# Kernel optimization log

Hardware: AMD Instinct MI355X
Metric: run time of the kernel (lower is better)

## Reference

```python
import jax, jax.numpy as jnp
import numpy as np

B, S, D, H = 4, 127, 768, 12
HD = D // H
NS = S + 1
GAMMA = 1.0
NEG_INF = -1e9
EPS = 1e-6


def setup_inputs() -> dict:
    key = jax.random.key(0)
    ks = jax.random.split(key, 12)
    s = 0.02
    return {
        'desc': jax.random.normal(ks[0], (B, S, D), jnp.float32),
        'nve': jax.random.normal(ks[1], (B, NS, D), jnp.float32),
        'mask_M': jax.random.uniform(ks[2], (B, H, S, S), jnp.float32),
        'Wq': jax.random.normal(ks[3], (D, D), jnp.float32) * s,
        'bq': jnp.zeros((D,), jnp.float32),
        'Wk': jax.random.normal(ks[4], (D, D), jnp.float32) * s,
        'bk': jnp.zeros((D,), jnp.float32),
        'Wv': jax.random.normal(ks[5], (D, D), jnp.float32) * s,
        'bv': jnp.zeros((D,), jnp.float32),
        'eW1': jax.random.normal(ks[6], (2 * D, D), jnp.float32) * s,
        'eb1': jnp.zeros((D,), jnp.float32),
        'ln_g': jnp.ones((D,), jnp.float32),
        'ln_b': jnp.zeros((D,), jnp.float32),
        'eW2': jax.random.normal(ks[7], (D, D), jnp.float32) * s,
        'eb2': jnp.zeros((D,), jnp.float32),
        'aW': jax.random.normal(ks[8], (3 * HD,), jnp.float32) * s,
        'ab': jnp.zeros((), jnp.float32),
    }


def _layernorm(x, g, b):
    m = jnp.mean(x, -1, keepdims=True)
    v = jnp.var(x, -1, keepdims=True)
    return (x - m) * jax.lax.rsqrt(v + 1e-5) * g + b


def _adjacency():
    # CLS->Var on, Var->CLS off, Var-Var without self loop
    var_adj = 1.0 - jnp.eye(S, dtype=jnp.float32)
    adj = jnp.zeros((NS, NS), jnp.float32)
    adj = adj.at[1:, 1:].set(var_adj)
    adj = adj.at[0, 1:].set(1.0)
    return adj  # [NS, NS]


def reference(desc, nve, mask_M, Wq, bq, Wk, bk, Wv, bv, eW1, eb1, ln_g, ln_b, eW2, eb2, aW, ab):
    adj = _adjacency()

    def proj(W, bias):
        return (nve @ W + bias).reshape(B, NS, H, HD).transpose(0, 2, 1, 3)  # [B,H,NS,HD]

    q, k, v = proj(Wq, bq), proj(Wk, bk), proj(Wv, bv)

    # edge features: pairwise concat of desc embeddings, CLS edges = [desc, desc]
    node_i = jnp.broadcast_to(desc[:, :, None, :], (B, S, S, D))
    node_j = jnp.broadcast_to(desc[:, None, :, :], (B, S, S, D))
    var_edge = jnp.concatenate([node_i, node_j], -1)           # [B,S,S,2D]
    cls_edge = jnp.concatenate([desc, desc], -1)               # [B,S,2D]
    edge = jnp.zeros((B, NS, NS, 2 * D), jnp.float32)
    edge = edge.at[:, 1:, 1:].set(var_edge)
    edge = edge.at[:, 0, 1:].set(cls_edge)
    edge = edge.at[:, 1:, 0].set(cls_edge)

    # edge_update MLP: Linear -> LayerNorm -> ReLU -> Linear
    h = jax.nn.relu(_layernorm(edge @ eW1 + eb1, ln_g, ln_b))
    e = h @ eW2 + eb2                                           # [B,NS,NS,D]
    e = e.reshape(B, NS, NS, H, HD).transpose(0, 3, 1, 2, 4)    # [B,H,NS,NS,HD]
    e = e * adj[None, None, :, :, None]

    # attn_proj on concat([q_i, k_j, e_ij]) == sum of three dot products + bias
    aq, ak, ae = aW[:HD], aW[HD:2 * HD], aW[2 * HD:]
    logits = (jnp.einsum('bhid,d->bhi', q, aq)[:, :, :, None]
              + jnp.einsum('bhjd,d->bhj', k, ak)[:, :, None, :]
              + jnp.einsum('bhijd,d->bhij', e, ae) + ab)        # [B,H,NS,NS]

    # logit bias from Var-Var probabilities
    p = jnp.clip(mask_M, EPS, 1.0 - EPS)
    bias = (jnp.log(p) - jnp.log(1.0 - p)) * GAMMA
    logits = logits.at[:, :, 1:, 1:].add(bias)

    logits = logits + jnp.where(adj == 0.0, NEG_INF, 0.0)[None, None]
    attn = jax.nn.softmax(logits, axis=-1)                      # dropout off (eval)
    context = jnp.einsum('bhij,bhjd->bhid', attn, v)
    basis_outputs = context.transpose(0, 2, 1, 3)               # [B,NS,H,HD]
    return basis_outputs, attn
```

## Files before the change

kernel.cpp:

```cpp
#include <hip/hip_runtime.h>
#include <hip/hip_bf16.h>

#define BB  4
#define SS  127
#define DD  768
#define HH  12
#define HDl 64
#define NSl 128

typedef __attribute__((ext_vector_type(8))) short short8;
typedef __attribute__((ext_vector_type(4))) float f32x4;

constexpr int OFF_P   = 0;
constexpr int OFF_Q   = OFF_P  + BB*SS*DD;
constexpr int OFF_V   = OFF_Q  + BB*SS*DD;
constexpr int OFF_QA  = OFF_V  + BB*NSl*DD;
constexpr int OFF_KA  = OFF_QA + BB*NSl*HH;
constexpr int OFF_W2B = OFF_KA + BB*NSl*HH;
constexpr int OFF_WQA = OFF_W2B + 6144;
constexpr int OFF_WKA = OFF_WQA + HH*DD;
constexpr int OFF_BF  = OFF_WKA + HH*DD;
constexpr int OFF_EL  = OFF_BF + 64;

__device__ inline unsigned short f2bf(float f) {
    unsigned int u = __builtin_bit_cast(unsigned int, f);
    u += 0x7fffu + ((u >> 16) & 1u);
    return (unsigned short)(u >> 16);
}

__device__ inline short8 pack8(float4 a, float4 b) {
    short8 p;
    p[0] = (short)f2bf(a.x); p[1] = (short)f2bf(a.y);
    p[2] = (short)f2bf(a.z); p[3] = (short)f2bf(a.w);
    p[4] = (short)f2bf(b.x); p[5] = (short)f2bf(b.y);
    p[6] = (short)f2bf(b.z); p[7] = (short)f2bf(b.w);
    return p;
}

__device__ inline void unpack8(short8 s, float* f) {
    int4 u = __builtin_bit_cast(int4, s);
    f[0] = __builtin_bit_cast(float, u.x << 16);
    f[1] = __builtin_bit_cast(float, u.x & 0xffff0000);
    f[2] = __builtin_bit_cast(float, u.y << 16);
    f[3] = __builtin_bit_cast(float, u.y & 0xffff0000);
    f[4] = __builtin_bit_cast(float, u.z << 16);
    f[5] = __builtin_bit_cast(float, u.z & 0xffff0000);
    f[6] = __builtin_bit_cast(float, u.w << 16);
    f[7] = __builtin_bit_cast(float, u.w & 0xffff0000);
}

__device__ inline unsigned int cvtpk(float lo, float hi) {
    unsigned int r;
    asm volatile("v_cvt_pk_bf16_f32 %0, %1, %2" : "=v"(r) : "v"(lo), "v"(hi));
    return r;
}

constexpr int NB_PQ   = 96;
constexpr int NB_V    = 96;
constexpr int FOLD_T  = 3 * HH * DD + 36 + 4 * DD;
constexpr int NB_FOLD = (FOLD_T + 511) / 512;

__global__ __launch_bounds__(512) void mega1(
        const float* __restrict__ desc, const float* __restrict__ nve,
        const float* __restrict__ eW1, const float* __restrict__ Wv,
        const float* __restrict__ bv, const float* __restrict__ eb1,
        const float* __restrict__ Wq, const float* __restrict__ Wk,
        const float* __restrict__ eW2,
        const float* __restrict__ bq, const float* __restrict__ bk,
        const float* __restrict__ eb2, const float* __restrict__ aW,
        unsigned short* __restrict__ Pu, unsigned short* __restrict__ Qu,
        unsigned short* __restrict__ Vu,
        unsigned short* __restrict__ W2Bu, float* __restrict__ WQA,
        float* __restrict__ WKA, float* __restrict__ bfold) {
    const int bid = blockIdx.x;
    const int tid = threadIdx.x;

    if (bid >= NB_PQ + NB_V) {
        int idx = (bid - NB_PQ - NB_V) * 512 + tid;
        const int total = 3 * HH * DD;
        if (idx < total) {
            int which = idx / (HH * DD);
            int r = idx % (HH * DD);
            int h = r / DD;
            int c = r % DD;
            const float* W = (which == 0) ? eW2 : (which == 1) ? Wq : Wk;
            const float* a = (which == 0) ? (aW + 2 * HDl) : (which == 1) ? aW : (aW + HDl);
            float s = 0.f;
            #pragma unroll 8
            for (int d = 0; d < HDl; ++d) s += W[c * DD + h * HDl + d] * a[d];
            if (which == 0) W2Bu[h * DD + c] = f2bf(s);
            else if (which == 1) WQA[h * DD + c] = s;
            else WKA[h * DD + c] = s;
        } else if (idx < total + 36) {
            int r = idx - total;
            int which = r / HH, h = r % HH;
            const float* bb = (which == 0) ? eb2 : (which == 1) ? bq : bk;
            const float* a = (which == 0) ? (aW + 2 * HDl) : (which == 1) ? aW : (aW + HDl);
            float s = 0.f;
            for (int d = 0; d < HDl; ++d) s += bb[h * HDl + d] * a[d];
            bfold[r] = s;
        } else if (idx < FOLD_T) {
            W2Bu[12 * DD + (idx - total - 36)] = 0;
        }
        return;
    }

    const bool pq = (bid < NB_PQ);
    const int r = pq ? bid : bid - NB_PQ;
    const int bcol = (r % 12) * 64;
    const int brow = (r / 12) * 64;
    const float* A  = pq ? desc : nve;
    const float* B0 = pq ? eW1 : Wv;
    const int M = pq ? (BB * SS) : (BB * NSl);

    __shared__ short lds[3 * 64 * 64];
    short* As  = lds;
    short* Bs0 = lds + 4096;
    short* Bs1 = lds + 8192;

    const int arow = tid >> 3, akc = (tid & 7) * 8;
    const int abyte = (arow * 128 + akc * 2) ^ ((arow & 7) << 4);
    const int bn = tid & 63, bg = tid >> 6;
    const int bbyte = (bn * 128 + bg * 16) ^ ((bn & 7) << 4);

    const int gm = brow + arow;
    const float* arow_p = A + gm * DD + akc;

    short8 gA, gB0, gB1;
    auto loadA = [&](int k0) {
        float4 f0 = {0,0,0,0}, f1 = {0,0,0,0};
        if (gm < M) {
            f0 = *(const float4*)(arow_p + k0);
            f1 = *(const float4*)(arow_p + k0 + 4);
        }
        gA = pack8(f0, f1);
    };
    auto loadB = [&](const float* Bm, int k0, short8& dst) {
        float v[8];
        #pragma unroll
        for (int q = 0; q < 8; ++q)
            v[q] = Bm[(k0 + bg * 8 + q) * DD + bcol + bn];
        short8 p;
        #pragma unroll
        for (int q = 0; q < 8; ++q) p[q] = (short)f2bf(v[q]);
        dst = p;
    };

    loadA(0);
    loadB(B0, 0, gB0);
    if (pq) loadB(eW1 + DD * DD, 0, gB1);

    const int lane = tid & 63;
    const int w = tid >> 6;
    const int wr = w >> 1, wc = w & 1;
    const int l15 = lane & 15;

    f32x4 acc0[2] = {};
    f32x4 acc1[2] = {};

    for (int k0 = 0; k0 < DD; k0 += 64) {
        *(short8*)((char*)As + abyte) = gA;
        *(short8*)((char*)Bs0 + bbyte) = gB0;
        if (pq) *(short8*)((char*)Bs1 + bbyte) = gB1;
        __syncthreads();
        if (k0 + 64 < DD) {
            loadA(k0 + 64);
            loadB(B0, k0 + 64, gB0);
            if (pq) loadB(eW1 + DD * DD, k0 + 64, gB1);
        }
        #pragma unroll
        for (int ks = 0; ks < 2; ++ks) {
            const int kb = ks * 64 + ((lane >> 4) << 4);
            int row = wr * 16 + l15;
            short8 af = *(const short8*)((char*)As + ((row * 128 + kb) ^ ((row & 7) << 4)));
            #pragma unroll
            for (int ni = 0; ni < 2; ++ni) {
                int col = wc * 32 + ni * 16 + l15;
                int cb = (col * 128 + kb) ^ ((col & 7) << 4);
                short8 b0 = *(const short8*)((char*)Bs0 + cb);
                acc0[ni] = __builtin_amdgcn_mfma_f32_16x16x32_bf16(af, b0, acc0[ni], 0, 0, 0);
                if (pq) {
                    short8 b1 = *(const short8*)((char*)Bs1 + cb);
                    acc1[ni] = __builtin_amdgcn_mfma_f32_16x16x32_bf16(af, b1, acc1[ni], 0, 0, 0);
                }
            }
        }
        __syncthreads();
    }

    #pragma unroll
    for (int ni = 0; ni < 2; ++ni) {
        int gcol = bcol + wc * 32 + ni * 16 + l15;
        float bias0 = pq ? 0.f : bv[gcol];
        float bias1 = pq ? eb1[gcol] : 0.f;
        #pragma unroll
        for (int rr = 0; rr < 4; ++rr) {
            int grow = brow + wr * 16 + ((lane >> 4) << 2) + rr;
            if (grow < M) {
                if (pq) {
                    Pu[grow * DD + gcol] = f2bf(acc0[ni][rr]);
                    Qu[grow * DD + gcol] = f2bf(acc1[ni][rr] + bias1);
                } else {
                    Vu[grow * DD + gcol] = f2bf(acc0[ni][rr] + bias0);
                }
            }
        }
    }
}

__global__ __launch_bounds__(512) void pairqk_kernel(
        const unsigned short* __restrict__ Pu, const unsigned short* __restrict__ Qu,
        const float* __restrict__ nve,
        const float* __restrict__ ln_g, const float* __restrict__ ln_b,
        const unsigned short* __restrict__ W2Bu,
        const float* __restrict__ WQA, const float* __restrict__ WKA,
        const float* __restrict__ bfold,
        float* __restrict__ qa, float* __restrict__ ka,
        float* __restrict__ e_log) {
    __shared__ short pB[16 * 768];
    __shared__ short qB[16 * 768];
    __shared__ float gbl[2 * 768];
    __shared__ float2 pstat[16];
    __shared__ float2 qstat[16];

    const int tid = threadIdx.x;

    if (blockIdx.z >= BB) {
        int qb = (blockIdx.z - BB) * 64 + blockIdx.y * 8 + blockIdx.x;
        int wid = qb * 8 + (tid >> 6);
        int lane = tid & 63;
        int which = wid & 1;
        int r = wid >> 1;
        int h = r % HH;
        int t = (r / HH) % NSl;
        int b = r / (HH * NSl);
        const float* W = (which ? WKA : WQA) + h * DD;
        const float* row = nve + (b * NSl + t) * DD;
        float s = 0.f;
        #pragma unroll
        for (int rr = 0; rr < 12; ++rr) {
            int c = lane + 64 * rr;
            s += row[c] * W[c];
        }
        #pragma unroll
        for (int off = 32; off; off >>= 1) s += __shfl_xor(s, off);
        if (lane == 0)
            (which ? ka : qa)[(b * NSl + t) * HH + h] = s + bfold[12 + which * 12 + h];
        return;
    }

    const int b   = blockIdx.z;
    const int pi0 = blockIdx.y * 16, qj0 = blockIdx.x * 16;

    {
        int row = tid >> 5;
        int ccb = tid & 31;
        const unsigned short* psrc = Pu + (b * SS + min(pi0 + row, SS - 1)) * DD;
        const unsigned short* qsrc = Qu + (b * SS + min(qj0 + row, SS - 1)) * DD;
        float ps = 0.f, pss = 0.f, qs = 0.f, qss = 0.f;
        float f[8];
        #pragma unroll
        for (int it = 0; it < 3; ++it) {
            int cc = ccb + it * 32;
            int byte = (row * 1536 + cc * 16) ^ ((row & 7) << 4);
            short8 pv = *(const short8*)(psrc + cc * 8);
            unpack8(pv, f);
            #pragma unroll
            for (int q = 0; q < 8; ++q) { ps += f[q]; pss += f[q] * f[q]; }
            *(short8*)((char*)pB + byte) = pv;
            short8 qv = *(const short8*)(qsrc + cc * 8);
            unpack8(qv, f);
            #pragma unroll
            for (int q = 0; q < 8; ++q) { qs += f[q]; qss += f[q] * f[q]; }
            *(short8*)((char*)qB + byte) = qv;
        }
        #pragma unroll
        for (int off = 16; off; off >>= 1) {
            ps  += __shfl_xor(ps, off);
            pss += __shfl_xor(pss, off);
            qs  += __shfl_xor(qs, off);
            qss += __shfl_xor(qss, off);
        }
        if ((tid & 31) == 0) {
            pstat[tid >> 5] = make_float2(ps, pss);
            qstat[tid >> 5] = make_float2(qs, qss);
        }
    }
    if (tid < 384) {
        int c = tid * 4;
        float4 v = (tid < 192) ? *(const float4*)(ln_g + c)
                               : *(const float4*)(ln_b + (c - 768));
        *(float4*)(gbl + c) = v;
    }
    __syncthreads();

    const int lane = tid & 63;
    const int w    = tid >> 6;
    const int l15  = lane & 15;
    const int kg   = lane >> 4;

    f32x4 gacc = {};
    #pragma unroll 4
    for (int ks = 0; ks < 24; ++ks) {
        int cb = ks * 64 + kg * 16;
        short8 ap = *(const short8*)((char*)pB + ((l15 * 1536 + cb) ^ ((l15 & 7) << 4)));
        short8 aq = *(const short8*)((char*)qB + ((l15 * 1536 + cb) ^ ((l15 & 7) << 4)));
        gacc = __builtin_amdgcn_mfma_f32_16x16x32_bf16(ap, aq, gacc, 0, 0, 0);
    }

    float al[2], be[2];
    #pragma unroll
    for (int s = 0; s < 2; ++s) {
        int pl = 2 * w + s;
        int src = ((pl >> 2) << 4) | l15;
        int rsel = pl & 3;
        float gg = (rsel == 0) ? gacc[0] : (rsel == 1) ? gacc[1]
                 : (rsel == 2) ? gacc[2] : gacc[3];
        gg = __shfl(gg, src);
        float2 pst = pstat[pl];
        float2 qst = qstat[l15];
        float mean = (pst.x + qst.x) * (1.f / DD);
        float sumsq = pst.y + 2.f * gg + qst.y;
        float var = sumsq * (1.f / DD) - mean * mean;
        float a = rsqrtf(var + 1e-5f);
        al[s] = a;
        be[s] = -mean * a;
    }

    const unsigned short* wrow = W2Bu + l15 * 768;
    const int r0 = 2 * w, r1 = 2 * w + 1;
    const int p0base = r0 * 1536, p1base = r1 * 1536;
    const int p0x = (r0 & 7) << 4, p1x = (r1 & 7) << 4;
    f32x4 acc0 = {}, acc1 = {};

    #pragma unroll 2
    for (int ks = 0; ks < 24; ++ks) {
        const int c0 = ks * 32 + kg * 8;
        short8 bfg = *(const short8*)(wrow + c0);
        f32x4 g0 = *(const f32x4*)(gbl + c0);
        f32x4 g1 = *(const f32x4*)(gbl + c0 + 4);
        f32x4 bb0 = *(const f32x4*)(gbl + 768 + c0);
        f32x4 bb1 = *(const f32x4*)(gbl + 768 + c0 + 4);
        float gv[8] = {g0.x, g0.y, g0.z, g0.w, g1.x, g1.y, g1.z, g1.w};
        float bv8[8] = {bb0.x, bb0.y, bb0.z, bb0.w, bb1.x, bb1.y, bb1.z, bb1.w};

        short8 q8 = *(const short8*)((char*)qB + ((l15 * 1536 + c0 * 2) ^ ((l15 & 7) << 4)));
        float qf[8];
        unpack8(q8, qf);

        short8 p8 = *(const short8*)((char*)pB + ((p0base + c0 * 2) ^ p0x));
        float pf[8];
        unpack8(p8, pf);
        float y[8];
        #pragma unroll
        for (int j = 0; j < 8; ++j) {
            float t = pf[j] + qf[j];
            float u = __builtin_fmaf(al[0], t, be[0]);
            y[j] = fmaxf(__builtin_fmaf(gv[j], u, bv8[j]), 0.f);
        }
        {
            int4 ti = { (int)cvtpk(y[0], y[1]), (int)cvtpk(y[2], y[3]),
                        (int)cvtpk(y[4], y[5]), (int)cvtpk(y[6], y[7]) };
            short8 ya = __builtin_bit_cast(short8, ti);
            acc0 = __builtin_amdgcn_mfma_f32_16x16x32_bf16(ya, bfg, acc0, 0, 0, 0);
        }

        p8 = *(const short8*)((char*)pB + ((p1base + c0 * 2) ^ p1x));
        unpack8(p8, pf);
        #pragma unroll
        for (int j = 0; j < 8; ++j) {
            float t = pf[j] + qf[j];
            float u = __builtin_fmaf(al[1], t, be[1]);
            y[j] = fmaxf(__builtin_fmaf(gv[j], u, bv8[j]), 0.f);
        }
        {
            int4 ti = { (int)cvtpk(y[0], y[1]), (int)cvtpk(y[2], y[3]),
                        (int)cvtpk(y[4], y[5]), (int)cvtpk(y[6], y[7]) };
            short8 ya = __builtin_bit_cast(short8, ti);
            acc1 = __builtin_amdgcn_mfma_f32_16x16x32_bf16(ya, bfg, acc1, 0, 0, 0);
        }
    }

    if (l15 < HH) {
        const float badd = bfold[l15];
        #pragma unroll
        for (int s = 0; s < 2; ++s) {
            int pig = pi0 + 2 * w + s;
            if (pig >= SS) continue;
            f32x4 A = s ? acc1 : acc0;
            #pragma unroll
            for (int r = 0; r < 4; ++r) {
                int qjg = qj0 + (kg << 2) + r;
                if (qjg < SS) {
                    int i = (pig == qjg) ? 0 : (pig + 1);
                    e_log[(((b * HH + l15) * NSl) + i) * NSl + (qjg + 1)] = A[r] + badd;
                }
            }
        }
    }
}

__global__ __launch_bounds__(512) void softmax_ctx_kernel(
        const float* __restrict__ e_log,
        const float* __restrict__ qa, const float* __restrict__ ka,
        const float* __restrict__ mask_M, const float* __restrict__ ab,
        const unsigned short* __restrict__ Vu,
        float* __restrict__ out) {
    __shared__ short Vt[64 * 128];
    __shared__ short plb[32 * 128];
    __shared__ float kal[NSl];

    const int b = blockIdx.z;
    const int h = blockIdx.y;
    const int iq = blockIdx.x;
    const int tid = threadIdx.x;
    const int lane = tid & 63;
    const int w = tid >> 6;

    {
        int j = tid >> 2;
        int dq = (tid & 3) * 16;
        const unsigned short* src = Vu + (b * NSl + j) * DD + h * HDl + dq;
        short8 s0 = *(const short8*)(src);
        short8 s1 = *(const short8*)(src + 8);
        #pragma unroll
        for (int t = 0; t < 8; ++t) {
            int d = dq + t;
            *(short*)((char*)Vt + ((d * 256 + j * 2) ^ ((d & 7) << 4))) = s0[t];
        }
        #pragma unroll
        for (int t = 0; t < 8; ++t) {
            int d = dq + 8 + t;
            *(short*)((char*)Vt + ((d * 256 + j * 2) ^ ((d & 7) << 4))) = s1[t];
        }
    }
    if (tid < NSl) kal[tid] = ka[(b * NSl + tid) * HH + h];
    __syncthreads();

    const float abv = ab[0];

    for (int rr = 0; rr < 4; ++rr) {
        const int il = w * 4 + rr;
        const int i = iq * 32 + il;
        const float qv = qa[(b * NSl + i) * HH + h];
        const float* e_row = e_log + (((b * HH + h) * NSl) + i) * NSl;

        float lg[2];
        bool valid[2];
        #pragma unroll
        for (int s = 0; s < 2; ++s) {
            int j = 1 + lane + 64 * s;
            bool v = (j < NSl) && !(i >= 1 && j == i);
            float l = -1e30f;
            if (v) {
                l = e_row[j] + qv + kal[j] + abv;
                if (i >= 1) {
                    float p = mask_M[((b * HH + h) * SS + (i - 1)) * SS + (j - 1)];
                    p = fminf(fmaxf(p, 1e-6f), 1.0f - 1e-6f);
                    l += __logf(p / (1.0f - p));
                }
            }
            lg[s] = l;
            valid[s] = v;
        }
        float m = fmaxf(lg[0], lg[1]);
        #pragma unroll
        for (int off = 32; off; off >>= 1) m = fmaxf(m, __shfl_xor(m, off));
        float e0 = valid[0] ? __expf(lg[0] - m) : 0.f;
        float e1 = valid[1] ? __expf(lg[1] - m) : 0.f;
        float s = e0 + e1;
        #pragma unroll
        for (int off = 32; off; off >>= 1) s += __shfl_xor(s, off);
        const float inv = 1.0f / s;

        const float p0 = e0 * inv, p1 = e1 * inv;

        float* attn_row = out + BB * NSl * HH * HDl + (((b * HH + h) * NSl) + i) * NSl;
        attn_row[1 + lane] = p0;
        if (65 + lane < NSl) attn_row[65 + lane] = p1;
        if (lane == 0) attn_row[0] = 0.f;

        {
            int byte0 = (il * 256 + (1 + lane) * 2) ^ ((il & 7) << 4);
            *(short*)((char*)plb + byte0) = (short)f2bf(p0);
            if (65 + lane < NSl) {
                int byte1 = (il * 256 + (65 + lane) * 2) ^ ((il & 7) << 4);
                *(short*)((char*)plb + byte1) = (short)f2bf(p1);
            }
            if (lane == 0) {
                int byteZ = (il * 256) ^ ((il & 7) << 4);
                *(short*)((char*)plb + byteZ) = 0;
            }
        }
    }
    __syncthreads();

    const int l15 = lane & 15;
    const int kg  = lane >> 4;
    const int itile = w >> 2, dtile = w & 3;
    const int arow  = itile * 16 + l15;
    const int bcold = dtile * 16 + l15;
    f32x4 acc = {};
    #pragma unroll
    for (int ks = 0; ks < 4; ++ks) {
        int kb = (ks * 32 + kg * 8) * 2;
        short8 af = *(const short8*)((char*)plb + ((arow * 256 + kb) ^ ((arow & 7) << 4)));
        short8 bf = *(const short8*)((char*)Vt  + ((bcold * 256 + kb) ^ ((bcold & 7) << 4)));
        acc = __builtin_amdgcn_mfma_f32_16x16x32_bf16(af, bf, acc, 0, 0, 0);
    }
    #pragma unroll
    for (int r = 0; r < 4; ++r) {
        int i = iq * 32 + itile * 16 + kg * 4 + r;
        out[((b * NSl + i) * HH + h) * HDl + dtile * 16 + l15] = acc[r];
    }
}

extern "C" void kernel_launch(void* const* d_in, const int* in_sizes, int n_in,
                              void* d_out, int out_size, void* d_ws, size_t ws_size,
                              hipStream_t stream) {
    const float* desc   = (const float*)d_in[0];
    const float* nve    = (const float*)d_in[1];
    const float* mask_M = (const float*)d_in[2];
    const float* Wq     = (const float*)d_in[3];
    const float* bq     = (const float*)d_in[4];
    const float* Wk     = (const float*)d_in[5];
    const float* bk     = (const float*)d_in[6];
    const float* Wv     = (const float*)d_in[7];
    const float* bv     = (const float*)d_in[8];
    const float* eW1    = (const float*)d_in[9];
    const float* eb1    = (const float*)d_in[10];
    const float* ln_g   = (const float*)d_in[11];
    const float* ln_b   = (const float*)d_in[12];
    const float* eW2    = (const float*)d_in[13];
    const float* eb2    = (const float*)d_in[14];
    const float* aW     = (const float*)d_in[15];
    const float* ab     = (const float*)d_in[16];

    float* ws  = (float*)d_ws;
    float* out = (float*)d_out;
    unsigned short* Pu   = (unsigned short*)(ws + OFF_P);
    unsigned short* Qu   = (unsigned short*)(ws + OFF_Q);
    unsigned short* Vu   = (unsigned short*)(ws + OFF_V);
    unsigned short* W2Bu = (unsigned short*)(ws + OFF_W2B);

    mega1<<<NB_PQ + NB_V + NB_FOLD, 512, 0, stream>>>(
        desc, nve, eW1, Wv, bv, eb1,
        Wq, Wk, eW2, bq, bk, eb2, aW,
        Pu, Qu, Vu,
        W2Bu, ws + OFF_WQA, ws + OFF_WKA, ws + OFF_BF);

    pairqk_kernel<<<dim3(8, 8, BB + 24), 512, 0, stream>>>(
        Pu, Qu, nve, ln_g, ln_b, W2Bu,
        ws + OFF_WQA, ws + OFF_WKA, ws + OFF_BF,
        ws + OFF_QA, ws + OFF_KA, ws + OFF_EL);

    softmax_ctx_kernel<<<dim3(4, HH, BB), 512, 0, stream>>>(
        ws + OFF_EL, ws + OFF_QA, ws + OFF_KA, mask_M, ab, Vu, out);
}
```

Before: 52.53 us.

## Double-buffer mega1 GEMM prefetch and split softmax_ctx into smaller blocks

```diff
diff --git a/kernel.cpp b/kernel.cpp
--- a/kernel.cpp
+++ b/kernel.cpp
@@ -111,12 +111,10 @@
     const int brow = (r / 12) * 64;
     const float* A  = pq ? desc : nve;
     const float* B0 = pq ? eW1 : Wv;
+    const float* B1 = eW1 + DD * DD;
     const int M = pq ? (BB * SS) : (BB * NSl);
 
-    __shared__ short lds[3 * 64 * 64];
-    short* As  = lds;
-    short* Bs0 = lds + 4096;
-    short* Bs1 = lds + 8192;
+    __shared__ short lds[2 * 3 * 4096];
 
     const int arow = tid >> 3, akc = (tid & 7) * 8;
     const int abyte = (arow * 128 + akc * 2) ^ ((arow & 7) << 4);
@@ -126,14 +124,13 @@
     const int gm = brow + arow;
     const float* arow_p = A + gm * DD + akc;
 
-    short8 gA, gB0, gB1;
-    auto loadA = [&](int k0) {
+    auto loadA = [&](int k0, short8& dst) {
         float4 f0 = {0,0,0,0}, f1 = {0,0,0,0};
         if (gm < M) {
             f0 = *(const float4*)(arow_p + k0);
             f1 = *(const float4*)(arow_p + k0 + 4);
         }
-        gA = pack8(f0, f1);
+        dst = pack8(f0, f1);
     };
     auto loadB = [&](const float* Bm, int k0, short8& dst) {
         float v[8];
@@ -146,9 +143,9 @@
         dst = p;
     };
 
-    loadA(0);
-    loadB(B0, 0, gB0);
-    if (pq) loadB(eW1 + DD * DD, 0, gB1);
+    short8 sA[2], sB0[2], sB1[2];
+    loadA(0, sA[0]);  loadB(B0, 0, sB0[0]);  if (pq) loadB(B1, 0, sB1[0]);
+    loadA(64, sA[1]); loadB(B0, 64, sB0[1]); if (pq) loadB(B1, 64, sB1[1]);
 
     const int lane = tid & 63;
     const int w = tid >> 6;
@@ -158,16 +155,24 @@
     f32x4 acc0[2] = {};
     f32x4 acc1[2] = {};
 
-    for (int k0 = 0; k0 < DD; k0 += 64) {
-        *(short8*)((char*)As + abyte) = gA;
-        *(short8*)((char*)Bs0 + bbyte) = gB0;
-        if (pq) *(short8*)((char*)Bs1 + bbyte) = gB1;
+    for (int k = 0; k < 12; ++k) {
+        const int p = k & 1;
+        short* As  = lds + p * 12288;
+        short* Bs0 = As + 4096;
+        short* Bs1 = As + 8192;
+
+        *(short8*)((char*)As + abyte)  = sA[p];
+        *(short8*)((char*)Bs0 + bbyte) = sB0[p];
+        if (pq) *(short8*)((char*)Bs1 + bbyte) = sB1[p];
         __syncthreads();
-        if (k0 + 64 < DD) {
-            loadA(k0 + 64);
-            loadB(B0, k0 + 64, gB0);
-            if (pq) loadB(eW1 + DD * DD, k0 + 64, gB1);
-        }
+
+        if (k + 2 < 12) {
+            int k0 = (k + 2) * 64;
+            loadA(k0, sA[p]);
+            loadB(B0, k0, sB0[p]);
+            if (pq) loadB(B1, k0, sB1[p]);
+        }
+
         #pragma unroll
         for (int ks = 0; ks < 2; ++ks) {
             const int kb = ks * 64 + ((lane >> 4) << 4);
@@ -400,14 +405,14 @@
     }
 }
 
-__global__ __launch_bounds__(512) void softmax_ctx_kernel(
+__global__ __launch_bounds__(256) void softmax_ctx_kernel(
         const float* __restrict__ e_log,
         const float* __restrict__ qa, const float* __restrict__ ka,
         const float* __restrict__ mask_M, const float* __restrict__ ab,
         const unsigned short* __restrict__ Vu,
         float* __restrict__ out) {
     __shared__ short Vt[64 * 128];
-    __shared__ short plb[32 * 128];
+    __shared__ short plb[16 * 128];
     __shared__ float kal[NSl];
 
     const int b = blockIdx.z;
@@ -418,20 +423,17 @@
     const int w = tid >> 6;
 
     {
-        int j = tid >> 2;
-        int dq = (tid & 3) * 16;
+        int j = tid >> 1;
+        int dq = (tid & 1) * 32;
         const unsigned short* src = Vu + (b * NSl + j) * DD + h * HDl + dq;
-        short8 s0 = *(const short8*)(src);
-        short8 s1 = *(const short8*)(src + 8);
-        #pragma unroll
-        for (int t = 0; t < 8; ++t) {
-            int d = dq + t;
-            *(short*)((char*)Vt + ((d * 256 + j * 2) ^ ((d & 7) << 4))) = s0[t];
-        }
-        #pragma unroll
-        for (int t = 0; t < 8; ++t) {
-            int d = dq + 8 + t;
-            *(short*)((char*)Vt + ((d * 256 + j * 2) ^ ((d & 7) << 4))) = s1[t];
+        #pragma unroll
+        for (int g = 0; g < 4; ++g) {
+            short8 s0 = *(const short8*)(src + g * 8);
+            #pragma unroll
+            for (int t = 0; t < 8; ++t) {
+                int d = dq + g * 8 + t;
+                *(short*)((char*)Vt + ((d * 256 + j * 2) ^ ((d & 7) << 4))) = s0[t];
+            }
         }
     }
     if (tid < NSl) kal[tid] = ka[(b * NSl + tid) * HH + h];
@@ -441,7 +443,7 @@
 
     for (int rr = 0; rr < 4; ++rr) {
         const int il = w * 4 + rr;
-        const int i = iq * 32 + il;
+        const int i = iq * 16 + il;
         const float qv = qa[(b * NSl + i) * HH + h];
         const float* e_row = e_log + (((b * HH + h) * NSl) + i) * NSl;
 
@@ -497,9 +499,8 @@
 
     const int l15 = lane & 15;
     const int kg  = lane >> 4;
-    const int itile = w >> 2, dtile = w & 3;
-    const int arow  = itile * 16 + l15;
-    const int bcold = dtile * 16 + l15;
+    const int arow  = l15;
+    const int bcold = w * 16 + l15;
     f32x4 acc = {};
     #pragma unroll
     for (int ks = 0; ks < 4; ++ks) {
@@ -510,8 +511,8 @@
     }
     #pragma unroll
     for (int r = 0; r < 4; ++r) {
-        int i = iq * 32 + itile * 16 + kg * 4 + r;
-        out[((b * NSl + i) * HH + h) * HDl + dtile * 16 + l15] = acc[r];
+        int i = iq * 16 + kg * 4 + r;
+        out[((b * NSl + i) * HH + h) * HDl + w * 16 + l15] = acc[r];
     }
 }
 
@@ -554,6 +555,6 @@
         ws + OFF_WQA, ws + OFF_WKA, ws + OFF_BF,
         ws + OFF_QA, ws + OFF_KA, ws + OFF_EL);
 
-    softmax_ctx_kernel<<<dim3(4, HH, BB), 512, 0, stream>>>(
+    softmax_ctx_kernel<<<dim3(8, HH, BB), 256, 0, stream>>>(
         ws + OFF_EL, ws + OFF_QA, ws + OFF_KA, mask_M, ab, Vu, out);
 }
```

Result: slower. 121.9 us (+132.0%).
